# Kernel tuning notes

Hardware: AMD Instinct MI355X
Metric: run time of the kernel (lower is better)

Reference implementation:

```python
import jax, jax.numpy as jnp
import numpy as np

B, A, R, I, V = 256, 196, 1024, 1024, 10000  # batch, att_size, rnn_size, input_size, output_size


def _lin_init(key, out_dim, in_dim):
    kw, kb = jax.random.split(key)
    s = 1.0 / np.sqrt(in_dim)
    w = jax.random.uniform(kw, (out_dim, in_dim), jnp.float32, -s, s)
    b = jax.random.uniform(kb, (out_dim,), jnp.float32, -s, s)
    return w, b


def setup_inputs() -> dict:
    key = jax.random.key(0)
    ks = jax.random.split(key, 11)
    x = jax.random.normal(ks[0], (B, I), jnp.float32)
    att = jax.random.normal(ks[1], (B, A, R), jnp.float32)
    prev_c = jax.random.normal(ks[2], (B, R), jnp.float32)
    prev_h = jax.random.normal(ks[3], (B, R), jnp.float32)
    a2a_w, a2a_b = _lin_init(ks[4], A, R)
    h2a_w, h2a_b = _lin_init(ks[5], A, R)
    d2d_w, d2d_b = _lin_init(ks[6], 1, A)
    i2h_w, i2h_b = _lin_init(ks[7], 4 * R, I)
    h2h_w, h2h_b = _lin_init(ks[8], 4 * R, R)
    r2a_w, r2a_b = _lin_init(ks[9], 4 * R, R)
    proj_w, proj_b = _lin_init(ks[10], V, R)
    return dict(x=x, att=att, prev_c=prev_c, prev_h=prev_h,
                a2a_w=a2a_w, a2a_b=a2a_b, h2a_w=h2a_w, h2a_b=h2a_b,
                d2d_w=d2d_w, d2d_b=d2d_b, i2h_w=i2h_w, i2h_b=i2h_b,
                h2h_w=h2h_w, h2h_b=h2h_b, r2a_w=r2a_w, r2a_b=r2a_b,
                proj_w=proj_w, proj_b=proj_b)


def reference(x, att, prev_c, prev_h, a2a_w, a2a_b, h2a_w, h2a_b,
              d2d_w, d2d_b, i2h_w, i2h_b, h2h_w, h2h_b,
              r2a_w, r2a_b, proj_w, proj_b):
    # Bahdanau-style attention: att [B, A, R]
    att_v = jnp.einsum('bir,ar->bia', att, a2a_w) + a2a_b      # [B, A, A]
    att_h = prev_h @ h2a_w.T + h2a_b                            # [B, A]
    dot = jnp.tanh(att_h[:, :, None] + att_v)                   # [B, A, A]
    score = jnp.einsum('bia,a->bi', dot, d2d_w[0]) + d2d_b[0]   # [B, A]
    weight = jax.nn.softmax(score, axis=1)                      # [B, A]
    att_res = jnp.einsum('bir,bi->br', att, weight)             # [B, R]
    # LSTM cell gating
    sums = (x @ i2h_w.T + i2h_b) + (prev_h @ h2h_w.T + h2h_b) + (att_res @ r2a_w.T + r2a_b)
    in_gate = jax.nn.sigmoid(sums[:, 0:R])
    forget_gate = jax.nn.sigmoid(sums[:, R:2 * R])
    out_gate = jax.nn.sigmoid(sums[:, 2 * R:3 * R])
    in_transform = jnp.tanh(sums[:, 3 * R:4 * R])
    next_c = forget_gate * prev_c + in_gate * in_transform
    next_h = out_gate * jnp.tanh(next_c)
    logsoft = jax.nn.log_softmax(next_h @ proj_w.T + proj_b, axis=1)
    return (next_c, next_h, logsoft)
```

## Files before the change

### kernel.cpp

```cpp
#include <hip/hip_runtime.h>
#include <math.h>

#define B_ 256
#define A_ 196
#define R_ 1024
#define V_ 10000
#define G4 4096
#define M_ (B_ * A_)

typedef __bf16 bf16x8 __attribute__((ext_vector_type(8)));
typedef float f32x4 __attribute__((ext_vector_type(4)));

#define OFF_ATTH   0
#define OFF_SCORE  50176
#define OFF_WEIGHT 100352
#define OFF_ATTRES 150528
#define OFF_P0     412672
#define OFF_P1     1461248
#define OFF_NHBF   2509824
#define OFF_LOGITS 2640896
#define OFF_PACKA  5200896
#define OFF_PACKH  5307392

__device__ __forceinline__ float tanh_fast(float x) {
    float e = __expf(2.f * x);
    return 1.f - 2.f / (e + 1.f);
}
__device__ __forceinline__ float sigmoid_fast(float x) {
    return 1.f / (1.f + __expf(-x));
}

__device__ __forceinline__ bf16x8 cvt8(float4 f0, float4 f1) {
    bf16x8 v;
    v[0] = (__bf16)f0.x; v[1] = (__bf16)f0.y; v[2] = (__bf16)f0.z; v[3] = (__bf16)f0.w;
    v[4] = (__bf16)f1.x; v[5] = (__bf16)f1.y; v[6] = (__bf16)f1.z; v[7] = (__bf16)f1.w;
    return v;
}

__global__ void pack_kernel(const float* __restrict__ a2a_w,
                            const float* __restrict__ h2a_w,
                            __bf16* __restrict__ packA,
                            __bf16* __restrict__ packH) {
    int row = blockIdx.x;
    int c = threadIdx.x * 4;
    if (row < 208) {
        float4 f = (row < A_) ? *(const float4*)(a2a_w + (size_t)row * R_ + c)
                              : make_float4(0.f, 0.f, 0.f, 0.f);
        __bf16* p = packA + (size_t)row * R_ + c;
        p[0] = (__bf16)f.x; p[1] = (__bf16)f.y; p[2] = (__bf16)f.z; p[3] = (__bf16)f.w;
    } else {
        int r2 = row - 208;
        float4 f = (r2 < A_) ? *(const float4*)(h2a_w + (size_t)r2 * R_ + c)
                             : make_float4(0.f, 0.f, 0.f, 0.f);
        __bf16* p = packH + (size_t)r2 * R_ + c;
        p[0] = (__bf16)f.x; p[1] = (__bf16)f.y; p[2] = (__bf16)f.z; p[3] = (__bf16)f.w;
    }
}

__global__ __launch_bounds__(256)
void att_h_gemm(const float* __restrict__ prev_h,
                const __bf16* __restrict__ packH,
                const float* __restrict__ h2a_b,
                float* __restrict__ att_h) {
    __shared__ alignas(16) __bf16 As[64][40];
    __shared__ alignas(16) __bf16 Bs[64][40];
    int tid = threadIdx.x;
    int m0 = blockIdx.x * 64, n0 = blockIdx.y * 64;
    int lane = tid & 63, w = tid >> 6, ln = lane & 15, quad = lane >> 4;
    int arow = tid >> 2, akq = (tid & 3) * 8;

    f32x4 acc[4];
#pragma unroll
    for (int t = 0; t < 4; ++t) acc[t] = {0.f, 0.f, 0.f, 0.f};

    const float* Asrc = prev_h + (size_t)(m0 + arow) * R_ + akq;
    const __bf16* Bsrc = packH + (size_t)(n0 + arow) * R_ + akq;

    float4 pa0 = *(const float4*)Asrc;
    float4 pa1 = *(const float4*)(Asrc + 4);
    bf16x8 pb = *(const bf16x8*)Bsrc;

    for (int k0 = 0; k0 < R_; k0 += 32) {
        __syncthreads();
        *(bf16x8*)&As[arow][akq] = cvt8(pa0, pa1);
        *(bf16x8*)&Bs[arow][akq] = pb;
        __syncthreads();
        if (k0 + 32 < R_) {
            pa0 = *(const float4*)(Asrc + k0 + 32);
            pa1 = *(const float4*)(Asrc + k0 + 36);
            pb = *(const bf16x8*)(Bsrc + k0 + 32);
        }
        bf16x8 a = *(bf16x8*)&As[w * 16 + ln][quad * 8];
#pragma unroll
        for (int t = 0; t < 4; ++t) {
            bf16x8 b = *(bf16x8*)&Bs[t * 16 + ln][quad * 8];
            acc[t] = __builtin_amdgcn_mfma_f32_16x16x32_bf16(a, b, acc[t], 0, 0, 0);
        }
    }
#pragma unroll
    for (int t = 0; t < 4; ++t) {
#pragma unroll
        for (int r = 0; r < 4; ++r) {
            int m = m0 + w * 16 + quad * 4 + r;
            int n = n0 + t * 16 + ln;
            if (n < A_) att_h[m * A_ + n] = acc[t][r] + h2a_b[n];
        }
    }
}

__global__ __launch_bounds__(256)
void score_gemm_mfma(const float* __restrict__ att,
                     const __bf16* __restrict__ packA,
                     const float* __restrict__ a2a_b,
                     const float* __restrict__ d2d_w,
                     const float* __restrict__ att_h,
                     float* __restrict__ score) {
    __shared__ alignas(16) __bf16 As[64][40];
    __shared__ alignas(16) __bf16 Bs[208][40];
    int tid = threadIdx.x;
    int m0 = blockIdx.x * 64;
    int lane = tid & 63, w = tid >> 6, ln = lane & 15, quad = lane >> 4;
    int arow = tid >> 2, akq = (tid & 3) * 8;

    f32x4 acc[13];
#pragma unroll
    for (int t = 0; t < 13; ++t) acc[t] = {0.f, 0.f, 0.f, 0.f};

    const float* Asrc = att + (size_t)(m0 + arow) * R_ + akq;

    float4 pa0 = *(const float4*)Asrc;
    float4 pa1 = *(const float4*)(Asrc + 4);
    bf16x8 pb[4];
#pragma unroll
    for (int i = 0; i < 4; ++i) {
        int c = tid + i * 256;
        if (c < 832) {
            int brow = c >> 2, bkq = (c & 3) * 8;
            pb[i] = *(const bf16x8*)(packA + (size_t)brow * R_ + bkq);
        }
    }

    for (int k0 = 0; k0 < R_; k0 += 32) {
        __syncthreads();
        *(bf16x8*)&As[arow][akq] = cvt8(pa0, pa1);
#pragma unroll
        for (int i = 0; i < 4; ++i) {
            int c = tid + i * 256;
            if (c < 832) {
                int brow = c >> 2, bkq = (c & 3) * 8;
                *(bf16x8*)&Bs[brow][bkq] = pb[i];
            }
        }
        __syncthreads();
        if (k0 + 32 < R_) {
            pa0 = *(const float4*)(Asrc + k0 + 32);
            pa1 = *(const float4*)(Asrc + k0 + 36);
#pragma unroll
            for (int i = 0; i < 4; ++i) {
                int c = tid + i * 256;
                if (c < 832) {
                    int brow = c >> 2, bkq = (c & 3) * 8;
                    pb[i] = *(const bf16x8*)(packA + (size_t)brow * R_ + k0 + 32 + bkq);
                }
            }
        }
        bf16x8 a = *(bf16x8*)&As[w * 16 + ln][quad * 8];
#pragma unroll
        for (int t = 0; t < 13; ++t) {
            bf16x8 b = *(bf16x8*)&Bs[t * 16 + ln][quad * 8];
            acc[t] = __builtin_amdgcn_mfma_f32_16x16x32_bf16(a, b, acc[t], 0, 0, 0);
        }
    }

    float wv[13], bb[13];
#pragma unroll
    for (int t = 0; t < 13; ++t) {
        int n = t * 16 + ln;
        wv[t] = (n < A_) ? d2d_w[n] : 0.f;
        bb[t] = (n < A_) ? a2a_b[n] : 0.f;
    }
#pragma unroll
    for (int r = 0; r < 4; ++r) {
        int m = m0 + w * 16 + quad * 4 + r;
        float ah = att_h[m];
        float p = 0.f;
#pragma unroll
        for (int t = 0; t < 13; ++t)
            p += tanh_fast(acc[t][r] + bb[t] + ah) * wv[t];
        p += __shfl_xor(p, 1);
        p += __shfl_xor(p, 2);
        p += __shfl_xor(p, 4);
        p += __shfl_xor(p, 8);
        if (ln == 0) score[m] = p;
    }
}

__global__ void softmax_kernel(const float* __restrict__ score,
                               const float* __restrict__ d2d_b,
                               float* __restrict__ weight) {
    int b = blockIdx.x;
    int i = threadIdx.x;
    __shared__ float red[256];
    float sval = 0.f;
    float s = -1e30f;
    if (i < A_) {
        sval = score[b * A_ + i] + d2d_b[0];
        s = sval;
    }
    red[i] = s; __syncthreads();
    for (int off = 128; off > 0; off >>= 1) {
        if (i < off) red[i] = fmaxf(red[i], red[i + off]);
        __syncthreads();
    }
    float mx = red[0]; __syncthreads();
    float e = (i < A_) ? __expf(sval - mx) : 0.f;
    red[i] = e; __syncthreads();
    for (int off = 128; off > 0; off >>= 1) {
        if (i < off) red[i] += red[i + off];
        __syncthreads();
    }
    float inv = 1.f / red[0];
    if (i < A_) weight[b * A_ + i] = e * inv;
}

__global__ __launch_bounds__(256)
void att_res_kernel(const float* __restrict__ att,
                    const float* __restrict__ weight,
                    float* __restrict__ att_res) {
    int b = blockIdx.x;
    int r = threadIdx.x * 4;
    __shared__ float w[A_];
    if (threadIdx.x < A_) w[threadIdx.x] = weight[b * A_ + threadIdx.x];
    __syncthreads();
    const float* ap = att + (size_t)b * A_ * R_ + r;
    float4 acc = make_float4(0.f, 0.f, 0.f, 0.f);
    for (int i = 0; i < A_; i += 4) {
        float4 v0 = *(const float4*)(ap + (size_t)(i + 0) * R_);
        float4 v1 = *(const float4*)(ap + (size_t)(i + 1) * R_);
        float4 v2 = *(const float4*)(ap + (size_t)(i + 2) * R_);
        float4 v3 = *(const float4*)(ap + (size_t)(i + 3) * R_);
        float w0 = w[i], w1 = w[i + 1], w2 = w[i + 2], w3 = w[i + 3];
        acc.x += v0.x * w0 + v1.x * w1 + v2.x * w2 + v3.x * w3;
        acc.y += v0.y * w0 + v1.y * w1 + v2.y * w2 + v3.y * w3;
        acc.z += v0.z * w0 + v1.z * w1 + v2.z * w2 + v3.z * w3;
        acc.w += v0.w * w0 + v1.w * w1 + v2.w * w2 + v3.w * w3;
    }
    *(float4*)(att_res + (size_t)b * R_ + r) = acc;
}

__global__ __launch_bounds__(256)
void sums_gemm_mfma(const float* __restrict__ x,
                    const float* __restrict__ prev_h,
                    const float* __restrict__ att_res,
                    const float* __restrict__ i2h_w,
                    const float* __restrict__ h2h_w,
                    const float* __restrict__ r2a_w,
                    float* __restrict__ P0,
                    float* __restrict__ P1) {
    __shared__ alignas(16) __bf16 As[64][40];
    __shared__ alignas(16) __bf16 Bs[64][40];
    int tid = threadIdx.x;
    int m0 = blockIdx.x * 64, n0 = blockIdx.y * 64;
    int ks = blockIdx.z;
    int kbeg = ks * 512, kend = kbeg + 512;
    int lane = tid & 63, w = tid >> 6, ln = lane & 15, quad = lane >> 4;
    int arow = tid >> 2, akq = (tid & 3) * 8;

    f32x4 acc[4];
#pragma unroll
    for (int t = 0; t < 4; ++t) acc[t] = {0.f, 0.f, 0.f, 0.f};

    const float* Al[3] = {x, prev_h, att_res};
    const float* Bl[3] = {i2h_w, h2h_w, r2a_w};
    for (int p = 0; p < 3; ++p) {
        const float* Asrc = Al[p] + (size_t)(m0 + arow) * R_ + akq;
        const float* Bsrc = Bl[p] + (size_t)(n0 + arow) * R_ + akq;
        float4 pa0 = *(const float4*)(Asrc + kbeg);
        float4 pa1 = *(const float4*)(Asrc + kbeg + 4);
        float4 pb0 = *(const float4*)(Bsrc + kbeg);
        float4 pb1 = *(const float4*)(Bsrc + kbeg + 4);
        for (int k0 = kbeg; k0 < kend; k0 += 32) {
            __syncthreads();
            *(bf16x8*)&As[arow][akq] = cvt8(pa0, pa1);
            *(bf16x8*)&Bs[arow][akq] = cvt8(pb0, pb1);
            __syncthreads();
            if (k0 + 32 < kend) {
                pa0 = *(const float4*)(Asrc + k0 + 32);
                pa1 = *(const float4*)(Asrc + k0 + 36);
                pb0 = *(const float4*)(Bsrc + k0 + 32);
                pb1 = *(const float4*)(Bsrc + k0 + 36);
            }
            bf16x8 a = *(bf16x8*)&As[w * 16 + ln][quad * 8];
#pragma unroll
            for (int t = 0; t < 4; ++t) {
                bf16x8 b = *(bf16x8*)&Bs[t * 16 + ln][quad * 8];
                acc[t] = __builtin_amdgcn_mfma_f32_16x16x32_bf16(a, b, acc[t], 0, 0, 0);
            }
        }
    }
    float* P = ks ? P1 : P0;
#pragma unroll
    for (int t = 0; t < 4; ++t) {
#pragma unroll
        for (int r = 0; r < 4; ++r) {
            int m = m0 + w * 16 + quad * 4 + r;
            int n = n0 + t * 16 + ln;
            P[(size_t)m * G4 + n] = acc[t][r];
        }
    }
}

__global__ void gates_kernel(const float* __restrict__ P0,
                             const float* __restrict__ P1,
                             const float* __restrict__ i2h_b,
                             const float* __restrict__ h2h_b,
                             const float* __restrict__ r2a_b,
                             const float* __restrict__ prev_c,
                             float* __restrict__ out_c,
                             float* __restrict__ out_h,
                             __bf16* __restrict__ nh_bf) {
    int idx = blockIdx.x * 256 + threadIdx.x;
    int b = idx >> 10, r = idx & 1023;
    size_t off = (size_t)b * G4;
    float s0 = P0[off + r] + P1[off + r] + i2h_b[r] + h2h_b[r] + r2a_b[r];
    float s1 = P0[off + R_ + r] + P1[off + R_ + r] + i2h_b[R_ + r] + h2h_b[R_ + r] + r2a_b[R_ + r];
    float s2 = P0[off + 2 * R_ + r] + P1[off + 2 * R_ + r] + i2h_b[2 * R_ + r] + h2h_b[2 * R_ + r] + r2a_b[2 * R_ + r];
    float s3 = P0[off + 3 * R_ + r] + P1[off + 3 * R_ + r] + i2h_b[3 * R_ + r] + h2h_b[3 * R_ + r] + r2a_b[3 * R_ + r];
    float ig = sigmoid_fast(s0);
    float fg = sigmoid_fast(s1);
    float og = sigmoid_fast(s2);
    float it = tanh_fast(s3);
    float nc = fg * prev_c[idx] + ig * it;
    float nh = og * tanh_fast(nc);
    out_c[idx] = nc;
    out_h[idx] = nh;
    nh_bf[idx] = (__bf16)nh;
}

__global__ __launch_bounds__(256)
void proj_gemm_mfma(const __bf16* __restrict__ nh_bf,
                    const float* __restrict__ proj_w,
                    const float* __restrict__ proj_b,
                    float* __restrict__ logits) {
    __shared__ alignas(16) __bf16 As[64][40];
    __shared__ alignas(16) __bf16 Bs[64][40];
    int tid = threadIdx.x;
    int m0 = blockIdx.x * 64, n0 = blockIdx.y * 64;
    int lane = tid & 63, w = tid >> 6, ln = lane & 15, quad = lane >> 4;
    int arow = tid >> 2, akq = (tid & 3) * 8;

    f32x4 acc[4];
#pragma unroll
    for (int t = 0; t < 4; ++t) acc[t] = {0.f, 0.f, 0.f, 0.f};

    int nr = n0 + arow;
    int nrc = nr < V_ ? nr : V_ - 1;
    const __bf16* Asrc = nh_bf + (size_t)(m0 + arow) * R_ + akq;
    const float* Bsrc = proj_w + (size_t)nrc * R_ + akq;

    bf16x8 pa = *(const bf16x8*)Asrc;
    float4 pb0 = *(const float4*)Bsrc;
    float4 pb1 = *(const float4*)(Bsrc + 4);

    for (int k0 = 0; k0 < R_; k0 += 32) {
        __syncthreads();
        *(bf16x8*)&As[arow][akq] = pa;
        *(bf16x8*)&Bs[arow][akq] = cvt8(pb0, pb1);
        __syncthreads();
        if (k0 + 32 < R_) {
            pa = *(const bf16x8*)(Asrc + k0 + 32);
            pb0 = *(const float4*)(Bsrc + k0 + 32);
            pb1 = *(const float4*)(Bsrc + k0 + 36);
        }
        bf16x8 a = *(bf16x8*)&As[w * 16 + ln][quad * 8];
#pragma unroll
        for (int t = 0; t < 4; ++t) {
            bf16x8 b = *(bf16x8*)&Bs[t * 16 + ln][quad * 8];
            acc[t] = __builtin_amdgcn_mfma_f32_16x16x32_bf16(a, b, acc[t], 0, 0, 0);
        }
    }
#pragma unroll
    for (int t = 0; t < 4; ++t) {
#pragma unroll
        for (int r = 0; r < 4; ++r) {
            int m = m0 + w * 16 + quad * 4 + r;
            int n = n0 + t * 16 + ln;
            if (n < V_) logits[(size_t)m * V_ + n] = acc[t][r] + proj_b[n];
        }
    }
}

__global__ void logsoftmax_kernel(const float* __restrict__ logits,
                                  float* __restrict__ out) {
    int b = blockIdx.x, t = threadIdx.x;
    __shared__ float red[256];
    const float* lp = logits + (size_t)b * V_;
    float mx = -1e30f;
    for (int v = t; v < V_; v += 256) mx = fmaxf(mx, lp[v]);
    red[t] = mx; __syncthreads();
    for (int off = 128; off > 0; off >>= 1) {
        if (t < off) red[t] = fmaxf(red[t], red[t + off]);
        __syncthreads();
    }
    mx = red[0]; __syncthreads();
    float s = 0.f;
    for (int v = t; v < V_; v += 256) s += __expf(lp[v] - mx);
    red[t] = s; __syncthreads();
    for (int off = 128; off > 0; off >>= 1) {
        if (t < off) red[t] += red[t + off];
        __syncthreads();
    }
    float lse = mx + __logf(red[0]);
    float* op = out + (size_t)b * V_;
    for (int v = t; v < V_; v += 256) op[v] = lp[v] - lse;
}

extern "C" void kernel_launch(void* const* d_in, const int* in_sizes, int n_in,
                              void* d_out, int out_size, void* d_ws, size_t ws_size,
                              hipStream_t stream) {
    const float* x      = (const float*)d_in[0];
    const float* att    = (const float*)d_in[1];
    const float* prev_c = (const float*)d_in[2];
    const float* prev_h = (const float*)d_in[3];
    const float* a2a_w  = (const float*)d_in[4];
    const float* a2a_b  = (const float*)d_in[5];
    const float* h2a_w  = (const float*)d_in[6];
    const float* h2a_b  = (const float*)d_in[7];
    const float* d2d_w  = (const float*)d_in[8];
    const float* d2d_b  = (const float*)d_in[9];
    const float* i2h_w  = (const float*)d_in[10];
    const float* i2h_b  = (const float*)d_in[11];
    const float* h2h_w  = (const float*)d_in[12];
    const float* h2h_b  = (const float*)d_in[13];
    const float* r2a_w  = (const float*)d_in[14];
    const float* r2a_b  = (const float*)d_in[15];
    const float* proj_w = (const float*)d_in[16];
    const float* proj_b = (const float*)d_in[17];

    float* ws      = (float*)d_ws;
    float* att_h   = ws + OFF_ATTH;
    float* score   = ws + OFF_SCORE;
    float* weight  = ws + OFF_WEIGHT;
    float* att_res = ws + OFF_ATTRES;
    float* P0      = ws + OFF_P0;
    float* P1      = ws + OFF_P1;
    __bf16* nh_bf  = (__bf16*)(ws + OFF_NHBF);
    float* logits  = ws + OFF_LOGITS;
    __bf16* packA  = (__bf16*)(ws + OFF_PACKA);
    __bf16* packH  = (__bf16*)(ws + OFF_PACKH);
    float* out     = (float*)d_out;

    pack_kernel<<<464, 256, 0, stream>>>(a2a_w, h2a_w, packA, packH);
    att_h_gemm<<<dim3(B_ / 64, 4), 256, 0, stream>>>(prev_h, packH, h2a_b, att_h);
    score_gemm_mfma<<<M_ / 64, 256, 0, stream>>>(att, packA, a2a_b, d2d_w, att_h, score);
    softmax_kernel<<<B_, 256, 0, stream>>>(score, d2d_b, weight);
    att_res_kernel<<<B_, 256, 0, stream>>>(att, weight, att_res);
    sums_gemm_mfma<<<dim3(B_ / 64, G4 / 64, 2), 256, 0, stream>>>(
        x, prev_h, att_res, i2h_w, h2h_w, r2a_w, P0, P1);
    gates_kernel<<<(B_ * R_) / 256, 256, 0, stream>>>(
        P0, P1, i2h_b, h2h_b, r2a_b, prev_c, out, out + B_ * R_, nh_bf);
    proj_gemm_mfma<<<dim3(B_ / 64, (V_ + 63) / 64), 256, 0, stream>>>(
        nh_bf, proj_w, proj_b, logits);
    logsoftmax_kernel<<<B_, 256, 0, stream>>>(logits, out + 2 * B_ * R_);
}
```

Baseline: 565.5 us.

## Retile score GEMM, split att_res, pre-pack proj weights, widen softmax

```diff
diff --git a/kernel.cpp b/kernel.cpp
--- a/kernel.cpp
+++ b/kernel.cpp
@@ -17,10 +17,12 @@
 #define OFF_ATTRES 150528
 #define OFF_P0     412672
 #define OFF_P1     1461248
-#define OFF_NHBF   2509824
-#define OFF_LOGITS 2640896
-#define OFF_PACKA  5200896
-#define OFF_PACKH  5307392
+#define OFF_P2     2509824
+#define OFF_NHBF   3558400
+#define OFF_LOGITS 3689472
+#define OFF_PACKA  6249472
+#define OFF_PACKH  6355968
+#define OFF_PACKP  6487040
 
 __device__ __forceinline__ float tanh_fast(float x) {
     float e = __expf(2.f * x);
@@ -39,22 +41,28 @@
 
 __global__ void pack_kernel(const float* __restrict__ a2a_w,
                             const float* __restrict__ h2a_w,
+                            const float* __restrict__ proj_w,
                             __bf16* __restrict__ packA,
-                            __bf16* __restrict__ packH) {
+                            __bf16* __restrict__ packH,
+                            __bf16* __restrict__ packP) {
     int row = blockIdx.x;
     int c = threadIdx.x * 4;
+    const float* src;
+    __bf16* dst;
     if (row < 208) {
-        float4 f = (row < A_) ? *(const float4*)(a2a_w + (size_t)row * R_ + c)
-                              : make_float4(0.f, 0.f, 0.f, 0.f);
-        __bf16* p = packA + (size_t)row * R_ + c;
-        p[0] = (__bf16)f.x; p[1] = (__bf16)f.y; p[2] = (__bf16)f.z; p[3] = (__bf16)f.w;
+        src = (row < A_) ? a2a_w + (size_t)row * R_ + c : nullptr;
+        dst = packA + (size_t)row * R_ + c;
+    } else if (row < 464) {
+        int r2 = row - 208;
+        src = (r2 < A_) ? h2a_w + (size_t)r2 * R_ + c : nullptr;
+        dst = packH + (size_t)r2 * R_ + c;
     } else {
-        int r2 = row - 208;
-        float4 f = (r2 < A_) ? *(const float4*)(h2a_w + (size_t)r2 * R_ + c)
-                             : make_float4(0.f, 0.f, 0.f, 0.f);
-        __bf16* p = packH + (size_t)r2 * R_ + c;
-        p[0] = (__bf16)f.x; p[1] = (__bf16)f.y; p[2] = (__bf16)f.z; p[3] = (__bf16)f.w;
-    }
+        int r3 = row - 464;
+        src = (r3 < V_) ? proj_w + (size_t)r3 * R_ + c : nullptr;
+        dst = packP + (size_t)r3 * R_ + c;
+    }
+    float4 f = src ? *(const float4*)src : make_float4(0.f, 0.f, 0.f, 0.f);
+    dst[0] = (__bf16)f.x; dst[1] = (__bf16)f.y; dst[2] = (__bf16)f.z; dst[3] = (__bf16)f.w;
 }
 
 __global__ __launch_bounds__(256)
@@ -117,82 +125,92 @@
                      float* __restrict__ score) {
     __shared__ alignas(16) __bf16 As[64][40];
     __shared__ alignas(16) __bf16 Bs[208][40];
+    __shared__ float sred[4][64];
     int tid = threadIdx.x;
     int m0 = blockIdx.x * 64;
     int lane = tid & 63, w = tid >> 6, ln = lane & 15, quad = lane >> 4;
     int arow = tid >> 2, akq = (tid & 3) * 8;
-
-    f32x4 acc[13];
-#pragma unroll
-    for (int t = 0; t < 13; ++t) acc[t] = {0.f, 0.f, 0.f, 0.f};
+    int nstart = (w == 0) ? 0 : 3 * w + 1;
+    int ncnt = (w == 0) ? 4 : 3;
+
+    f32x4 acc[4][4];
+#pragma unroll
+    for (int mt = 0; mt < 4; ++mt)
+#pragma unroll
+        for (int t = 0; t < 4; ++t) acc[mt][t] = {0.f, 0.f, 0.f, 0.f};
 
     const float* Asrc = att + (size_t)(m0 + arow) * R_ + akq;
-
-    float4 pa0 = *(const float4*)Asrc;
-    float4 pa1 = *(const float4*)(Asrc + 4);
-    bf16x8 pb[4];
-#pragma unroll
-    for (int i = 0; i < 4; ++i) {
-        int c = tid + i * 256;
-        if (c < 832) {
-            int brow = c >> 2, bkq = (c & 3) * 8;
-            pb[i] = *(const bf16x8*)(packA + (size_t)brow * R_ + bkq);
-        }
-    }
-
-    for (int k0 = 0; k0 < R_; k0 += 32) {
-        __syncthreads();
-        *(bf16x8*)&As[arow][akq] = cvt8(pa0, pa1);
-#pragma unroll
-        for (int i = 0; i < 4; ++i) {
-            int c = tid + i * 256;
-            if (c < 832) {
-                int brow = c >> 2, bkq = (c & 3) * 8;
-                *(bf16x8*)&Bs[brow][bkq] = pb[i];
+    const __bf16* Bb = packA + (size_t)arow * R_ + akq;
+
+    float4 pa0[2], pa1[2];
+    pa0[0] = *(const float4*)(Asrc);      pa1[0] = *(const float4*)(Asrc + 4);
+    pa0[1] = *(const float4*)(Asrc + 32); pa1[1] = *(const float4*)(Asrc + 36);
+    bf16x8 pbv[4];
+#pragma unroll
+    for (int i = 0; i < 4; ++i)
+        if (i < 3 || arow < 16) pbv[i] = *(const bf16x8*)(Bb + (size_t)i * 64 * R_);
+
+    for (int it = 0; it < 32; ++it) {
+        int k0 = it * 32;
+        int p = it & 1;
+        __syncthreads();
+        *(bf16x8*)&As[arow][akq] = cvt8(pa0[p], pa1[p]);
+        *(bf16x8*)&Bs[arow][akq] = pbv[0];
+        *(bf16x8*)&Bs[arow + 64][akq] = pbv[1];
+        *(bf16x8*)&Bs[arow + 128][akq] = pbv[2];
+        if (arow < 16) *(bf16x8*)&Bs[arow + 192][akq] = pbv[3];
+        __syncthreads();
+        if (k0 + 64 < R_) {
+            pa0[p] = *(const float4*)(Asrc + k0 + 64);
+            pa1[p] = *(const float4*)(Asrc + k0 + 68);
+        }
+        if (k0 + 32 < R_) {
+#pragma unroll
+            for (int i = 0; i < 4; ++i)
+                if (i < 3 || arow < 16)
+                    pbv[i] = *(const bf16x8*)(Bb + (size_t)i * 64 * R_ + k0 + 32);
+        }
+        bf16x8 af[4];
+#pragma unroll
+        for (int mt = 0; mt < 4; ++mt) af[mt] = *(bf16x8*)&As[mt * 16 + ln][quad * 8];
+#pragma unroll
+        for (int t = 0; t < 4; ++t) {
+            if (t < ncnt) {
+                bf16x8 b = *(bf16x8*)&Bs[(nstart + t) * 16 + ln][quad * 8];
+#pragma unroll
+                for (int mt = 0; mt < 4; ++mt)
+                    acc[mt][t] = __builtin_amdgcn_mfma_f32_16x16x32_bf16(af[mt], b, acc[mt][t], 0, 0, 0);
             }
         }
-        __syncthreads();
-        if (k0 + 32 < R_) {
-            pa0 = *(const float4*)(Asrc + k0 + 32);
-            pa1 = *(const float4*)(Asrc + k0 + 36);
-#pragma unroll
-            for (int i = 0; i < 4; ++i) {
-                int c = tid + i * 256;
-                if (c < 832) {
-                    int brow = c >> 2, bkq = (c & 3) * 8;
-                    pb[i] = *(const bf16x8*)(packA + (size_t)brow * R_ + k0 + 32 + bkq);
-                }
-            }
-        }
-        bf16x8 a = *(bf16x8*)&As[w * 16 + ln][quad * 8];
-#pragma unroll
-        for (int t = 0; t < 13; ++t) {
-            bf16x8 b = *(bf16x8*)&Bs[t * 16 + ln][quad * 8];
-            acc[t] = __builtin_amdgcn_mfma_f32_16x16x32_bf16(a, b, acc[t], 0, 0, 0);
-        }
-    }
-
-    float wv[13], bb[13];
-#pragma unroll
-    for (int t = 0; t < 13; ++t) {
-        int n = t * 16 + ln;
-        wv[t] = (n < A_) ? d2d_w[n] : 0.f;
-        bb[t] = (n < A_) ? a2a_b[n] : 0.f;
-    }
-#pragma unroll
-    for (int r = 0; r < 4; ++r) {
-        int m = m0 + w * 16 + quad * 4 + r;
-        float ah = att_h[m];
-        float p = 0.f;
-#pragma unroll
-        for (int t = 0; t < 13; ++t)
-            p += tanh_fast(acc[t][r] + bb[t] + ah) * wv[t];
-        p += __shfl_xor(p, 1);
-        p += __shfl_xor(p, 2);
-        p += __shfl_xor(p, 4);
-        p += __shfl_xor(p, 8);
-        if (ln == 0) score[m] = p;
-    }
+    }
+
+    float wv[4], bb[4];
+#pragma unroll
+    for (int t = 0; t < 4; ++t) {
+        int n = (nstart + t) * 16 + ln;
+        bool v = (t < ncnt) && (n < A_);
+        wv[t] = v ? d2d_w[n] : 0.f;
+        bb[t] = v ? a2a_b[n] : 0.f;
+    }
+#pragma unroll
+    for (int mt = 0; mt < 4; ++mt) {
+#pragma unroll
+        for (int r = 0; r < 4; ++r) {
+            int row = mt * 16 + quad * 4 + r;
+            float ah = att_h[m0 + row];
+            float pp = 0.f;
+#pragma unroll
+            for (int t = 0; t < 4; ++t)
+                if (t < ncnt) pp += tanh_fast(acc[mt][t][r] + bb[t] + ah) * wv[t];
+            pp += __shfl_xor(pp, 1);
+            pp += __shfl_xor(pp, 2);
+            pp += __shfl_xor(pp, 4);
+            pp += __shfl_xor(pp, 8);
+            if (ln == 0) sred[w][row] = pp;
+        }
+    }
+    __syncthreads();
+    if (tid < 64) score[m0 + tid] = sred[0][tid] + sred[1][tid] + sred[2][tid] + sred[3][tid];
 }
 
 __global__ void softmax_kernel(const float* __restrict__ score,
@@ -228,24 +246,28 @@
                     const float* __restrict__ weight,
                     float* __restrict__ att_res) {
     int b = blockIdx.x;
+    int seg = blockIdx.y;
     int r = threadIdx.x * 4;
-    __shared__ float w[A_];
-    if (threadIdx.x < A_) w[threadIdx.x] = weight[b * A_ + threadIdx.x];
+    __shared__ float w[49];
+    int i0 = seg * 49;
+    if (threadIdx.x < 49) w[threadIdx.x] = weight[b * A_ + i0 + threadIdx.x];
     __syncthreads();
-    const float* ap = att + (size_t)b * A_ * R_ + r;
+    const float* ap = att + ((size_t)b * A_ + i0) * R_ + r;
     float4 acc = make_float4(0.f, 0.f, 0.f, 0.f);
-    for (int i = 0; i < A_; i += 4) {
-        float4 v0 = *(const float4*)(ap + (size_t)(i + 0) * R_);
-        float4 v1 = *(const float4*)(ap + (size_t)(i + 1) * R_);
-        float4 v2 = *(const float4*)(ap + (size_t)(i + 2) * R_);
-        float4 v3 = *(const float4*)(ap + (size_t)(i + 3) * R_);
-        float w0 = w[i], w1 = w[i + 1], w2 = w[i + 2], w3 = w[i + 3];
-        acc.x += v0.x * w0 + v1.x * w1 + v2.x * w2 + v3.x * w3;
-        acc.y += v0.y * w0 + v1.y * w1 + v2.y * w2 + v3.y * w3;
-        acc.z += v0.z * w0 + v1.z * w1 + v2.z * w2 + v3.z * w3;
-        acc.w += v0.w * w0 + v1.w * w1 + v2.w * w2 + v3.w * w3;
-    }
-    *(float4*)(att_res + (size_t)b * R_ + r) = acc;
+    for (int i = 0; i < 49; i += 7) {
+#pragma unroll
+        for (int j = 0; j < 7; ++j) {
+            float4 v = *(const float4*)(ap + (size_t)(i + j) * R_);
+            float ww = w[i + j];
+            acc.x += v.x * ww; acc.y += v.y * ww;
+            acc.z += v.z * ww; acc.w += v.w * ww;
+        }
+    }
+    float* dst = att_res + (size_t)b * R_ + r;
+    atomicAdd(dst + 0, acc.x);
+    atomicAdd(dst + 1, acc.y);
+    atomicAdd(dst + 2, acc.z);
+    atomicAdd(dst + 3, acc.w);
 }
 
 __global__ __launch_bounds__(256)
@@ -256,13 +278,13 @@
                     const float* __restrict__ h2h_w,
                     const float* __restrict__ r2a_w,
                     float* __restrict__ P0,
-                    float* __restrict__ P1) {
+                    float* __restrict__ P1,
+                    float* __restrict__ P2) {
     __shared__ alignas(16) __bf16 As[64][40];
     __shared__ alignas(16) __bf16 Bs[64][40];
     int tid = threadIdx.x;
     int m0 = blockIdx.x * 64, n0 = blockIdx.y * 64;
-    int ks = blockIdx.z;
-    int kbeg = ks * 512, kend = kbeg + 512;
+    int z = blockIdx.z;
     int lane = tid & 63, w = tid >> 6, ln = lane & 15, quad = lane >> 4;
     int arow = tid >> 2, akq = (tid & 3) * 8;
 
@@ -272,33 +294,33 @@
 
     const float* Al[3] = {x, prev_h, att_res};
     const float* Bl[3] = {i2h_w, h2h_w, r2a_w};
-    for (int p = 0; p < 3; ++p) {
-        const float* Asrc = Al[p] + (size_t)(m0 + arow) * R_ + akq;
-        const float* Bsrc = Bl[p] + (size_t)(n0 + arow) * R_ + akq;
-        float4 pa0 = *(const float4*)(Asrc + kbeg);
-        float4 pa1 = *(const float4*)(Asrc + kbeg + 4);
-        float4 pb0 = *(const float4*)(Bsrc + kbeg);
-        float4 pb1 = *(const float4*)(Bsrc + kbeg + 4);
-        for (int k0 = kbeg; k0 < kend; k0 += 32) {
-            __syncthreads();
-            *(bf16x8*)&As[arow][akq] = cvt8(pa0, pa1);
-            *(bf16x8*)&Bs[arow][akq] = cvt8(pb0, pb1);
-            __syncthreads();
-            if (k0 + 32 < kend) {
-                pa0 = *(const float4*)(Asrc + k0 + 32);
-                pa1 = *(const float4*)(Asrc + k0 + 36);
-                pb0 = *(const float4*)(Bsrc + k0 + 32);
-                pb1 = *(const float4*)(Bsrc + k0 + 36);
-            }
-            bf16x8 a = *(bf16x8*)&As[w * 16 + ln][quad * 8];
-#pragma unroll
-            for (int t = 0; t < 4; ++t) {
-                bf16x8 b = *(bf16x8*)&Bs[t * 16 + ln][quad * 8];
-                acc[t] = __builtin_amdgcn_mfma_f32_16x16x32_bf16(a, b, acc[t], 0, 0, 0);
-            }
-        }
-    }
-    float* P = ks ? P1 : P0;
+    float* Pl[3] = {P0, P1, P2};
+    const float* Asrc = Al[z] + (size_t)(m0 + arow) * R_ + akq;
+    const float* Bsrc = Bl[z] + (size_t)(n0 + arow) * R_ + akq;
+
+    float4 pa0 = *(const float4*)Asrc;
+    float4 pa1 = *(const float4*)(Asrc + 4);
+    float4 pb0 = *(const float4*)Bsrc;
+    float4 pb1 = *(const float4*)(Bsrc + 4);
+    for (int k0 = 0; k0 < R_; k0 += 32) {
+        __syncthreads();
+        *(bf16x8*)&As[arow][akq] = cvt8(pa0, pa1);
+        *(bf16x8*)&Bs[arow][akq] = cvt8(pb0, pb1);
+        __syncthreads();
+        if (k0 + 32 < R_) {
+            pa0 = *(const float4*)(Asrc + k0 + 32);
+            pa1 = *(const float4*)(Asrc + k0 + 36);
+            pb0 = *(const float4*)(Bsrc + k0 + 32);
+            pb1 = *(const float4*)(Bsrc + k0 + 36);
+        }
+        bf16x8 a = *(bf16x8*)&As[w * 16 + ln][quad * 8];
+#pragma unroll
+        for (int t = 0; t < 4; ++t) {
+            bf16x8 b = *(bf16x8*)&Bs[t * 16 + ln][quad * 8];
+            acc[t] = __builtin_amdgcn_mfma_f32_16x16x32_bf16(a, b, acc[t], 0, 0, 0);
+        }
+    }
+    float* P = Pl[z];
 #pragma unroll
     for (int t = 0; t < 4; ++t) {
 #pragma unroll
@@ -312,6 +334,7 @@
 
 __global__ void gates_kernel(const float* __restrict__ P0,
                              const float* __restrict__ P1,
+                             const float* __restrict__ P2,
                              const float* __restrict__ i2h_b,
                              const float* __restrict__ h2h_b,
                              const float* __restrict__ r2a_b,
@@ -322,10 +345,14 @@
     int idx = blockIdx.x * 256 + threadIdx.x;
     int b = idx >> 10, r = idx & 1023;
     size_t off = (size_t)b * G4;
-    float s0 = P0[off + r] + P1[off + r] + i2h_b[r] + h2h_b[r] + r2a_b[r];
-    float s1 = P0[off + R_ + r] + P1[off + R_ + r] + i2h_b[R_ + r] + h2h_b[R_ + r] + r2a_b[R_ + r];
-    float s2 = P0[off + 2 * R_ + r] + P1[off + 2 * R_ + r] + i2h_b[2 * R_ + r] + h2h_b[2 * R_ + r] + r2a_b[2 * R_ + r];
-    float s3 = P0[off + 3 * R_ + r] + P1[off + 3 * R_ + r] + i2h_b[3 * R_ + r] + h2h_b[3 * R_ + r] + r2a_b[3 * R_ + r];
+    float s0 = P0[off + r] + P1[off + r] + P2[off + r]
+             + i2h_b[r] + h2h_b[r] + r2a_b[r];
+    float s1 = P0[off + R_ + r] + P1[off + R_ + r] + P2[off + R_ + r]
+             + i2h_b[R_ + r] + h2h_b[R_ + r] + r2a_b[R_ + r];
+    float s2 = P0[off + 2 * R_ + r] + P1[off + 2 * R_ + r] + P2[off + 2 * R_ + r]
+             + i2h_b[2 * R_ + r] + h2h_b[2 * R_ + r] + r2a_b[2 * R_ + r];
+    float s3 = P0[off + 3 * R_ + r] + P1[off + 3 * R_ + r] + P2[off + 3 * R_ + r]
+             + i2h_b[3 * R_ + r] + h2h_b[3 * R_ + r] + r2a_b[3 * R_ + r];
     float ig = sigmoid_fast(s0);
     float fg = sigmoid_fast(s1);
     float og = sigmoid_fast(s2);
@@ -339,7 +366,7 @@
 
 __global__ __launch_bounds__(256)
 void proj_gemm_mfma(const __bf16* __restrict__ nh_bf,
-                    const float* __restrict__ proj_w,
+                    const __bf16* __restrict__ packP,
                     const float* __restrict__ proj_b,
                     float* __restrict__ logits) {
     __shared__ alignas(16) __bf16 As[64][40];
@@ -353,25 +380,23 @@
 #pragma unroll
     for (int t = 0; t < 4; ++t) acc[t] = {0.f, 0.f, 0.f, 0.f};
 
-    int nr = n0 + arow;
-    int nrc = nr < V_ ? nr : V_ - 1;
     const __bf16* Asrc = nh_bf + (size_t)(m0 + arow) * R_ + akq;
-    const float* Bsrc = proj_w + (size_t)nrc * R_ + akq;
+    const __bf16* Bsrc = packP + (size_t)(n0 + arow) * R_ + akq;
 
     bf16x8 pa = *(const bf16x8*)Asrc;
-    float4 pb0 = *(const float4*)Bsrc;
-    float4 pb1 = *(const float4*)(Bsrc + 4);
-
-    for (int k0 = 0; k0 < R_; k0 += 32) {
+    bf16x8 pb[2];
+    pb[0] = *(const bf16x8*)Bsrc;
+    pb[1] = *(const bf16x8*)(Bsrc + 32);
+
+    for (int it = 0; it < 32; ++it) {
+        int k0 = it * 32;
+        int p = it & 1;
         __syncthreads();
         *(bf16x8*)&As[arow][akq] = pa;
-        *(bf16x8*)&Bs[arow][akq] = cvt8(pb0, pb1);
-        __syncthreads();
-        if (k0 + 32 < R_) {
-            pa = *(const bf16x8*)(Asrc + k0 + 32);
-            pb0 = *(const float4*)(Bsrc + k0 + 32);
-            pb1 = *(const float4*)(Bsrc + k0 + 36);
-        }
+        *(bf16x8*)&Bs[arow][akq] = pb[p];
+        __syncthreads();
+        if (k0 + 32 < R_) pa = *(const bf16x8*)(Asrc + k0 + 32);
+        if (k0 + 64 < R_) pb[p] = *(const bf16x8*)(Bsrc + k0 + 64);
         bf16x8 a = *(bf16x8*)&As[w * 16 + ln][quad * 8];
 #pragma unroll
         for (int t = 0; t < 4; ++t) {
@@ -390,29 +415,30 @@
     }
 }
 
-__global__ void logsoftmax_kernel(const float* __restrict__ logits,
-                                  float* __restrict__ out) {
+__global__ __launch_bounds__(1024)
+void logsoftmax_kernel(const float* __restrict__ logits,
+                       float* __restrict__ out) {
     int b = blockIdx.x, t = threadIdx.x;
-    __shared__ float red[256];
+    __shared__ float red[1024];
     const float* lp = logits + (size_t)b * V_;
     float mx = -1e30f;
-    for (int v = t; v < V_; v += 256) mx = fmaxf(mx, lp[v]);
+    for (int v = t; v < V_; v += 1024) mx = fmaxf(mx, lp[v]);
     red[t] = mx; __syncthreads();
-    for (int off = 128; off > 0; off >>= 1) {
+    for (int off = 512; off > 0; off >>= 1) {
         if (t < off) red[t] = fmaxf(red[t], red[t + off]);
         __syncthreads();
     }
     mx = red[0]; __syncthreads();
     float s = 0.f;
-    for (int v = t; v < V_; v += 256) s += __expf(lp[v] - mx);
+    for (int v = t; v < V_; v += 1024) s += __expf(lp[v] - mx);
     red[t] = s; __syncthreads();
-    for (int off = 128; off > 0; off >>= 1) {
+    for (int off = 512; off > 0; off >>= 1) {
         if (t < off) red[t] += red[t + off];
         __syncthreads();
     }
     float lse = mx + __logf(red[0]);
     float* op = out + (size_t)b * V_;
-    for (int v = t; v < V_; v += 256) op[v] = lp[v] - lse;
+    for (int v = t; v < V_; v += 1024) op[v] = lp[v] - lse;
 }
 
 extern "C" void kernel_launch(void* const* d_in, const int* in_sizes, int n_in,
@@ -444,22 +470,25 @@
     float* att_res = ws + OFF_ATTRES;
     float* P0      = ws + OFF_P0;
     float* P1      = ws + OFF_P1;
+    float* P2      = ws + OFF_P2;
     __bf16* nh_bf  = (__bf16*)(ws + OFF_NHBF);
     float* logits  = ws + OFF_LOGITS;
     __bf16* packA  = (__bf16*)(ws + OFF_PACKA);
     __bf16* packH  = (__bf16*)(ws + OFF_PACKH);
+    __bf16* packP  = (__bf16*)(ws + OFF_PACKP);
     float* out     = (float*)d_out;
 
-    pack_kernel<<<464, 256, 0, stream>>>(a2a_w, h2a_w, packA, packH);
+    hipMemsetAsync(att_res, 0, B_ * R_ * sizeof(float), stream);
+    pack_kernel<<<10512, 256, 0, stream>>>(a2a_w, h2a_w, proj_w, packA, packH, packP);
     att_h_gemm<<<dim3(B_ / 64, 4), 256, 0, stream>>>(prev_h, packH, h2a_b, att_h);
     score_gemm_mfma<<<M_ / 64, 256, 0, stream>>>(att, packA, a2a_b, d2d_w, att_h, score);
     softmax_kernel<<<B_, 256, 0, stream>>>(score, d2d_b, weight);
-    att_res_kernel<<<B_, 256, 0, stream>>>(att, weight, att_res);
-    sums_gemm_mfma<<<dim3(B_ / 64, G4 / 64, 2), 256, 0, stream>>>(
-        x, prev_h, att_res, i2h_w, h2h_w, r2a_w, P0, P1);
+    att_res_kernel<<<dim3(B_, 4), 256, 0, stream>>>(att, weight, att_res);
+    sums_gemm_mfma<<<dim3(B_ / 64, G4 / 64, 3), 256, 0, stream>>>(
+        x, prev_h, att_res, i2h_w, h2h_w, r2a_w, P0, P1, P2);
     gates_kernel<<<(B_ * R_) / 256, 256, 0, stream>>>(
-        P0, P1, i2h_b, h2h_b, r2a_b, prev_c, out, out + B_ * R_, nh_bf);
+        P0, P1, P2, i2h_b, h2h_b, r2a_b, prev_c, out, out + B_ * R_, nh_bf);
     proj_gemm_mfma<<<dim3(B_ / 64, (V_ + 63) / 64), 256, 0, stream>>>(
-        nh_bf, proj_w, proj_b, logits);
-    logsoftmax_kernel<<<B_, 256, 0, stream>>>(logits, out + 2 * B_ * R_);
-}
+        nh_bf, packP, proj_b, logits);
+    logsoftmax_kernel<<<B_, 1024, 0, stream>>>(logits, out + 2 * B_ * R_);
+}
```

Result: slower. 718.5 us (+27.1%).
